# Kernel tuning notes

Measured on AMD Instinct MI355X. Metric: run time of the kernel, lower is better.

The kernel has to match this reference:

```python
import jax, jax.numpy as jnp
import numpy as np

NUM_USERS = 50000
NUM_FOODS = 20000
USER_FEAT_DIM = 256
FOOD_FEAT_DIM = 256
EMBED_DIM = 128
NUM_LAYERS = 3
NUM_HEADS = 4
THRESHOLD = 0.3
E_UF = 600000  # user->food interactions; symmetrized to 2*E_UF directed edges


def setup_inputs() -> dict:
    key = jax.random.key(0)
    ks = jax.random.split(key, 12)
    user_feat = jax.random.normal(ks[0], (NUM_USERS, USER_FEAT_DIM), jnp.float32)
    food_feat = jax.random.normal(ks[1], (NUM_FOODS, FOOD_FEAT_DIM), jnp.float32)
    # bipartite edges in global index space, symmetrized (both directions)
    u = jax.random.randint(ks[2], (E_UF,), 0, NUM_USERS)
    f = jax.random.randint(ks[3], (E_UF,), 0, NUM_FOODS) + NUM_USERS
    edge_index = jnp.stack([jnp.concatenate([u, f]), jnp.concatenate([f, u])]).astype(jnp.int64)
    s = 0.02
    W_user = jax.random.normal(ks[4], (USER_FEAT_DIM, EMBED_DIM), jnp.float32) * s
    b_user = jnp.zeros((EMBED_DIM,), jnp.float32)
    W_food = jax.random.normal(ks[5], (FOOD_FEAT_DIM, EMBED_DIM), jnp.float32) * s
    b_food = jnp.zeros((EMBED_DIM,), jnp.float32)
    Wq = jax.random.normal(ks[6], (EMBED_DIM, EMBED_DIM), jnp.float32) * s
    Wk = jax.random.normal(ks[7], (EMBED_DIM, EMBED_DIM), jnp.float32) * s
    channel_weights = jnp.zeros((2,), jnp.float32)  # StructurePooling fusion weights
    user_embed = jax.random.normal(ks[8], (NUM_USERS, EMBED_DIM), jnp.float32) * 0.1
    item_embed = jax.random.normal(ks[9], (NUM_FOODS, EMBED_DIM), jnp.float32) * 0.1
    return {"user_feat": user_feat, "food_feat": food_feat, "edge_index": edge_index,
            "W_user": W_user, "b_user": b_user, "W_food": W_food, "b_food": b_food,
            "Wq": Wq, "Wk": Wk, "channel_weights": channel_weights,
            "user_embed": user_embed, "item_embed": item_embed}


def reference(user_feat, food_feat, edge_index, W_user, b_user, W_food, b_food,
              Wq, Wk, channel_weights, user_embed, item_embed):
    N = NUM_USERS + NUM_FOODS
    Dh = EMBED_DIM // NUM_HEADS
    # feature projections + relu
    user_emb = jax.nn.relu(user_feat @ W_user + b_user)   # [U, D]
    food_emb = jax.nn.relu(food_feat @ W_food + b_food)   # [F, D]
    row, col = edge_index[0], edge_index[1]
    # graph generator: per-edge multi-head cosine similarity between user/food endpoints
    u_idx = jnp.where(row < NUM_USERS, row, col)
    f_idx = jnp.where(row < NUM_USERS, col, row) - NUM_USERS
    q = (user_emb[u_idx] @ Wq).reshape(-1, NUM_HEADS, Dh)  # [E, H, Dh]
    k = (food_emb[f_idx] @ Wk).reshape(-1, NUM_HEADS, Dh)
    eps = 1e-8
    sim = (q * k).sum(-1) / (jnp.linalg.norm(q, axis=-1) * jnp.linalg.norm(k, axis=-1) + eps)
    mask_feature = (sim.mean(-1) > THRESHOLD).astype(jnp.float32)  # [E]
    # structure pooling fusion of [all-ones, feature mask]
    w = jax.nn.softmax(channel_weights)
    fused = w[0] * 1.0 + w[1] * mask_feature
    edge_mask = (fused > 0.5).astype(jnp.float32)
    # LightGCN: symmetric-normalized propagation on the masked graph
    deg = jnp.maximum(jax.ops.segment_sum(edge_mask, row, num_segments=N), 1.0)
    norm = edge_mask / jnp.sqrt(deg[row] * deg[col])       # [E]
    x0 = jnp.concatenate([user_embed, item_embed], axis=0)  # [N, D]
    x = x0
    acc = x0
    for _ in range(NUM_LAYERS):
        x = jax.ops.segment_sum(norm[:, None] * x[col], row, num_segments=N)
        acc = acc + x
    out = acc / float(NUM_LAYERS + 1)
    return (out[:NUM_USERS], out[NUM_USERS:], user_embed, item_embed)
```

## Files before the change

kernel.cpp:

```cpp
#include <hip/hip_runtime.h>
#include <cstdint>

#define U_NUM 50000
#define F_NUM 20000
#define N_NUM 70000
#define D_EMB 128
#define THRESH 0.3f

typedef _Float16 half8 __attribute__((ext_vector_type(8)));
typedef float f32x4 __attribute__((ext_vector_type(4)));
typedef unsigned short u16x8 __attribute__((ext_vector_type(8)));

#define NRT_U ((U_NUM + 127) / 128)
#define NRT_F ((F_NUM + 127) / 128)
#define GRID_U (((NRT_U + 7) / 8) * 16)
#define GRID_F (((NRT_F + 7) / 8) * 16)

__device__ __forceinline__ void map_tile(int lb, int nRT, int& rt, int& ch, bool& valid)
{
    int g = lb >> 4, o = lb & 15;
    ch = (o >> 3) & 1;
    rt = g * 8 + (o & 7);
    valid = (rt < nRT);
}

__device__ __forceinline__ void gl_lds16(const void* g, void* l)
{
    __builtin_amdgcn_global_load_lds(
        (const __attribute__((address_space(1))) unsigned int*)g,
        (__attribute__((address_space(3))) unsigned int*)l, 16, 0, 0);
}

__global__ void presplit_zero(const float* __restrict__ Wu, const float* __restrict__ Wf,
                              const float* __restrict__ Wq, const float* __restrict__ Wk,
                              unsigned short* __restrict__ dst,
                              int* __restrict__ cnt, int* __restrict__ cursor)
{
    int i = blockIdx.x * 256 + threadIdx.x;
    if (i < N_NUM) { cnt[i] = 0; cursor[i] = 0; }
    if (i >= 98304) return;
    float a; size_t d; int pstride;
    if (i < 32768) {
        int n = i >> 8, k = i & 255;
        a = Wu[k * 128 + n]; d = (size_t)n * 256 + k; pstride = 32768;
    } else if (i < 65536) {
        int j = i - 32768; int n = j >> 8, k = j & 255;
        a = Wf[k * 128 + n]; d = 65536 + (size_t)n * 256 + k; pstride = 32768;
    } else if (i < 81920) {
        int j = i - 65536; int n = j >> 7, k = j & 127;
        a = Wq[k * 128 + n]; d = 131072 + (size_t)n * 128 + k; pstride = 16384;
    } else {
        int j = i - 81920; int n = j >> 7, k = j & 127;
        a = Wk[k * 128 + n]; d = 163840 + (size_t)n * 128 + k; pstride = 16384;
    }
    _Float16 c1 = (_Float16)a;
    float r = a - (float)c1;
    _Float16 c2 = (_Float16)r;
    dst[d]           = __builtin_bit_cast(unsigned short, c1);
    dst[d + pstride] = __builtin_bit_cast(unsigned short, c2);
}

__device__ __forceinline__ void split2v(const f32x4 x0, const f32x4 x1,
                                        half8& h, half8& lo)
{
    float v[8] = {x0[0], x0[1], x0[2], x0[3], x1[0], x1[1], x1[2], x1[3]};
#pragma unroll
    for (int i = 0; i < 8; i++) {
        _Float16 c1 = (_Float16)v[i];
        h[i] = c1;
        lo[i] = (_Float16)(v[i] - (float)c1);
    }
}

__global__ __launch_bounds__(256, 3)
void gemm1(const float* __restrict__ uf, const float* __restrict__ ff,
           const unsigned short* __restrict__ Wsp,
           const float* __restrict__ bu, const float* __restrict__ bfo,
           unsigned short* __restrict__ Eh)
{
    __shared__ char lds[49152];

    unsigned short* El = Eh + (size_t)N_NUM * 128;
    const int bid = blockIdx.x;
    const bool isU = bid < GRID_U;
    const int lb = isU ? bid : bid - GRID_U;
    int rt, chf; bool valid;
    map_tile(lb, isU ? NRT_U : NRT_F, rt, chf, valid);
    if (!valid) return;
    const int n0 = chf * 64;
    const int Mloc = isU ? U_NUM : F_NUM;
    const int combBase = isU ? 0 : U_NUM;
    const float* A  = isU ? uf : ff;
    const float* b1 = isU ? bu : bfo;
    const unsigned short* W = Wsp + (isU ? 0 : 65536);

    const int tid = threadIdx.x;
    const int w  = tid >> 6;
    const int l  = tid & 63;
    const int lm = l & 15;
    const int lq = l >> 4;
    const int wr = w * 32;

    auto stage = [&](int b, int kc) {
#pragma unroll
        for (int j = 0; j < 4; ++j) {
            int off = w * 4096 + j * 1024 + l * 16;
            int row = off >> 7;
            int ch  = (off & 127) >> 4;
            int gch = ch ^ (row & 7);
            int gr  = min(rt * 128 + row, Mloc - 1);
            const float* src = A + (size_t)gr * 256 + kc * 32 + gch * 4;
            gl_lds16(src, lds + b * 16384 + w * 4096 + j * 1024);
        }
#pragma unroll
        for (int j = 0; j < 2; ++j) {
            int off = w * 2048 + j * 1024 + l * 16;
            int p   = off >> 12;
            int n   = (off & 4095) >> 6;
            int ch  = (off & 63) >> 4;
            int gch = ch ^ ((n >> 1) & 3);
            const unsigned short* src = W + (size_t)p * 32768 + (size_t)(n0 + n) * 256 + kc * 32 + gch * 8;
            gl_lds16(src, lds + 32768 + b * 8192 + w * 2048 + j * 1024);
        }
    };

    stage(0, 0);
    __syncthreads();

    f32x4 acc[2][4];
#pragma unroll
    for (int i = 0; i < 2; i++)
#pragma unroll
        for (int j = 0; j < 4; j++) acc[i][j] = (f32x4)0.f;

    int buf = 0;
#pragma unroll
    for (int kc = 0; kc < 8; ++kc) {
        if (kc < 7) stage(buf ^ 1, kc + 1);

        half8 ah[2], al[2];
#pragma unroll
        for (int rb = 0; rb < 2; ++rb) {
            int lr = wr + rb * 16 + lm;
            int r7 = lr & 7;
            const float* basep = (const float*)(lds + buf * 16384 + lr * 128);
            f32x4 x0 = *(const f32x4*)(basep + ((((lq * 2)     ) ^ r7) << 2));
            f32x4 x1 = *(const f32x4*)(basep + ((((lq * 2) + 1) ^ r7) << 2));
            split2v(x0, x1, ah[rb], al[rb]);
        }
#pragma unroll
        for (int cb = 0; cb < 4; ++cb) {
            int n = cb * 16 + lm;
            int wc = lq ^ ((n >> 1) & 3);
            const char* wbase = lds + 32768 + buf * 8192;
            half8 bh = *(const half8*)(wbase + n * 64 + wc * 16);
            half8 bl = *(const half8*)(wbase + 4096 + n * 64 + wc * 16);
#pragma unroll
            for (int rb = 0; rb < 2; ++rb) {
                acc[rb][cb] = __builtin_amdgcn_mfma_f32_16x16x32_f16(al[rb], bh, acc[rb][cb], 0, 0, 0);
                acc[rb][cb] = __builtin_amdgcn_mfma_f32_16x16x32_f16(ah[rb], bl, acc[rb][cb], 0, 0, 0);
                acc[rb][cb] = __builtin_amdgcn_mfma_f32_16x16x32_f16(ah[rb], bh, acc[rb][cb], 0, 0, 0);
            }
        }
        __syncthreads();
        buf ^= 1;
    }

#pragma unroll
    for (int cb = 0; cb < 4; ++cb) {
        const int col = n0 + cb * 16 + lm;
        const float bb = b1[col];
#pragma unroll
        for (int rb = 0; rb < 2; ++rb)
#pragma unroll
            for (int rg = 0; rg < 4; ++rg) {
                int lr = wr + rb * 16 + lq * 4 + rg;
                if (rt * 128 + lr < Mloc) {
                    size_t rr = (size_t)(combBase + rt * 128 + lr);
                    float e = fmaxf(acc[rb][cb][rg] + bb, 0.f);
                    _Float16 c1 = (_Float16)e;
                    _Float16 c2 = (_Float16)(e - (float)c1);
                    Eh[rr * 128 + col] = __builtin_bit_cast(unsigned short, c1);
                    El[rr * 128 + col] = __builtin_bit_cast(unsigned short, c2);
                }
            }
    }
}

__global__ __launch_bounds__(256, 3)
void gemm2(const unsigned short* __restrict__ Eh,
           const unsigned short* __restrict__ Wsp,
           float* __restrict__ Qo, unsigned short* __restrict__ QKh)
{
    __shared__ char lds[49152];

    const unsigned short* El = Eh + (size_t)N_NUM * 128;
    const int bid = blockIdx.x;
    const bool isU = bid < GRID_U;
    const int lb = isU ? bid : bid - GRID_U;
    int rt, chf; bool valid;
    map_tile(lb, isU ? NRT_U : NRT_F, rt, chf, valid);
    if (!valid) return;
    const int n0 = chf * 64;
    const int Mloc = isU ? U_NUM : F_NUM;
    const int combBase = isU ? 0 : U_NUM;
    const unsigned short* W = Wsp + (isU ? 131072 : 163840);

    const int tid = threadIdx.x;
    const int w  = tid >> 6;
    const int l  = tid & 63;
    const int lm = l & 15;
    const int lq = l >> 4;
    const int wr = w * 32;

    auto stage = [&](int b, int kc) {
#pragma unroll
        for (int j = 0; j < 4; ++j) {
            int off = w * 4096 + j * 1024 + l * 16;
            int p   = off >> 13;
            int ro  = (off & 8191) >> 6;
            int ch  = (off & 63) >> 4;
            int gch = ch ^ ((ro >> 1) & 3);
            int gr  = min(rt * 128 + ro, Mloc - 1) + combBase;
            const unsigned short* src = (p ? El : Eh) + (size_t)gr * 128 + kc * 32 + gch * 8;
            gl_lds16(src, lds + b * 16384 + w * 4096 + j * 1024);
        }
#pragma unroll
        for (int j = 0; j < 2; ++j) {
            int off = w * 2048 + j * 1024 + l * 16;
            int p   = off >> 12;
            int n   = (off & 4095) >> 6;
            int ch  = (off & 63) >> 4;
            int gch = ch ^ ((n >> 1) & 3);
            const unsigned short* src = W + (size_t)p * 16384 + (size_t)(n0 + n) * 128 + kc * 32 + gch * 8;
            gl_lds16(src, lds + 32768 + b * 8192 + w * 2048 + j * 1024);
        }
    };

    stage(0, 0);
    __syncthreads();

    f32x4 acc[2][4];
#pragma unroll
    for (int i = 0; i < 2; i++)
#pragma unroll
        for (int j = 0; j < 4; j++) acc[i][j] = (f32x4)0.f;

    int buf = 0;
#pragma unroll
    for (int kc = 0; kc < 4; ++kc) {
        if (kc < 3) stage(buf ^ 1, kc + 1);

        half8 ah[2], al[2];
#pragma unroll
        for (int rb = 0; rb < 2; ++rb) {
            int lr = wr + rb * 16 + lm;
            int ech = lq ^ ((lr >> 1) & 3);
            const char* eb = lds + buf * 16384;
            ah[rb] = *(const half8*)(eb + lr * 64 + ech * 16);
            al[rb] = *(const half8*)(eb + 8192 + lr * 64 + ech * 16);
        }
#pragma unroll
        for (int cb = 0; cb < 4; ++cb) {
            int n = cb * 16 + lm;
            int wc = lq ^ ((n >> 1) & 3);
            const char* wbase = lds + 32768 + buf * 8192;
            half8 bh = *(const half8*)(wbase + n * 64 + wc * 16);
            half8 bl = *(const half8*)(wbase + 4096 + n * 64 + wc * 16);
#pragma unroll
            for (int rb = 0; rb < 2; ++rb) {
                acc[rb][cb] = __builtin_amdgcn_mfma_f32_16x16x32_f16(al[rb], bh, acc[rb][cb], 0, 0, 0);
                acc[rb][cb] = __builtin_amdgcn_mfma_f32_16x16x32_f16(ah[rb], bl, acc[rb][cb], 0, 0, 0);
                acc[rb][cb] = __builtin_amdgcn_mfma_f32_16x16x32_f16(ah[rb], bh, acc[rb][cb], 0, 0, 0);
            }
        }
        __syncthreads();
        buf ^= 1;
    }

#pragma unroll
    for (int cb = 0; cb < 4; ++cb) {
        const int col = n0 + cb * 16 + lm;
#pragma unroll
        for (int rb = 0; rb < 2; ++rb)
#pragma unroll
            for (int rg = 0; rg < 4; ++rg) {
                int lr = wr + rb * 16 + lq * 4 + rg;
                if (rt * 128 + lr < Mloc) {
                    size_t rr = (size_t)(combBase + rt * 128 + lr);
                    float v = acc[rb][cb][rg];
                    Qo[rr * 128 + col] = v;
                    QKh[rr * 128 + col] = __builtin_bit_cast(unsigned short, (_Float16)v);
                }
            }
    }
}

__global__ __launch_bounds__(256)
void edge_kernel(const int* __restrict__ ei, int Edir,
                 const unsigned short* __restrict__ QKh, const float* __restrict__ QKf,
                 const float* __restrict__ cwts,
                 float* __restrict__ maskf, int* __restrict__ cnt, int Eund)
{
    int gid = blockIdx.x * 256 + threadIdx.x;
    int e = gid >> 3;
    if (e >= Eund) return;
    int sub = gid & 7;
    int row = ei[e];
    int col = ei[Edir + e];
    row = min(max(row, 0), N_NUM - 1);
    col = min(max(col, 0), N_NUM - 1);
    int u  = (row < U_NUM) ? row : col;
    int fg = (row < U_NUM) ? col : row;
    u = min(max(u, 0), U_NUM - 1);
    int f = min(max(fg - U_NUM, 0), F_NUM - 1);
    const size_t qrow = (size_t)u * D_EMB;
    const size_t krow = (size_t)(U_NUM + f) * D_EMB;

    const unsigned short* qh = QKh + qrow + sub * 16;
    const unsigned short* kh = QKh + krow + sub * 16;
    u16x8 qa = *(const u16x8*)(qh);
    u16x8 qb = *(const u16x8*)(qh + 8);
    u16x8 ka = *(const u16x8*)(kh);
    u16x8 kb = *(const u16x8*)(kh + 8);
    float dot = 0.f, qq = 0.f, kk = 0.f;
#pragma unroll
    for (int i = 0; i < 8; i++) {
        float qv = (float)__builtin_bit_cast(_Float16, (unsigned short)qa[i]);
        float kv = (float)__builtin_bit_cast(_Float16, (unsigned short)ka[i]);
        dot += qv * kv; qq += qv * qv; kk += kv * kv;
    }
#pragma unroll
    for (int i = 0; i < 8; i++) {
        float qv = (float)__builtin_bit_cast(_Float16, (unsigned short)qb[i]);
        float kv = (float)__builtin_bit_cast(_Float16, (unsigned short)kb[i]);
        dot += qv * kv; qq += qv * qv; kk += kv * kv;
    }
    dot += __shfl_xor(dot, 1);
    qq  += __shfl_xor(qq, 1);
    kk  += __shfl_xor(kk, 1);
    float denom = sqrtf(qq) * sqrtf(kk) + 1e-8f;
    float sim = dot / denom;
    float s = sim + __shfl_xor(sim, 2);
    s += __shfl_xor(s, 4);
    float mean = s * 0.25f;

    if (fabsf(mean - THRESH) < 0.03f) {
        const float4* qp = (const float4*)(QKf + qrow + sub * 16);
        const float4* kp = (const float4*)(QKf + krow + sub * 16);
        float dot2 = 0.f, qq2 = 0.f, kk2 = 0.f;
#pragma unroll
        for (int i = 0; i < 4; i++) {
            float4 a = qp[i]; float4 b = kp[i];
            dot2 += a.x * b.x + a.y * b.y + a.z * b.z + a.w * b.w;
            qq2  += a.x * a.x + a.y * a.y + a.z * a.z + a.w * a.w;
            kk2  += b.x * b.x + b.y * b.y + b.z * b.z + b.w * b.w;
        }
        dot2 += __shfl_xor(dot2, 1);
        qq2  += __shfl_xor(qq2, 1);
        kk2  += __shfl_xor(kk2, 1);
        float denom2 = sqrtf(qq2) * sqrtf(kk2) + 1e-8f;
        float sim2 = dot2 / denom2;
        float s2 = sim2 + __shfl_xor(sim2, 2);
        s2 += __shfl_xor(s2, 4);
        mean = s2 * 0.25f;
    }

    float mf = (mean > THRESH) ? 1.f : 0.f;
    float cw0 = cwts[0], cw1 = cwts[1];
    float mx = fmaxf(cw0, cw1);
    float e0 = expf(cw0 - mx), e1 = expf(cw1 - mx);
    float inv = 1.f / (e0 + e1);
    float fused = e0 * inv + (e1 * inv) * mf;
    float em = (fused > 0.5f) ? 1.f : 0.f;

    if (sub == 0) {
        maskf[e] = em;
        if (em != 0.f) {
            atomicAdd(&cnt[row], 1);
            atomicAdd(&cnt[col], 1);
        }
    }
}

__global__ void scan_part(const int* __restrict__ cnt, int* __restrict__ part, int n)
{
    __shared__ int sd[256];
    int b = blockIdx.x, t = threadIdx.x;
    int base = b * 1024;
    int s = 0;
#pragma unroll
    for (int j = 0; j < 4; j++) {
        int idx = base + t + j * 256;
        if (idx < n) s += cnt[idx];
    }
    sd[t] = s; __syncthreads();
    for (int d = 128; d > 0; d >>= 1) {
        if (t < d) sd[t] += sd[t + d];
        __syncthreads();
    }
    if (t == 0) part[b] = sd[0];
}

__global__ void scan_small(int* part, int nb)
{
    __shared__ int sd[256];
    int t = threadIdx.x;
    sd[t] = (t < nb) ? part[t] : 0;
    __syncthreads();
    for (int d = 1; d < 256; d <<= 1) {
        int x = (t >= d) ? sd[t - d] : 0;
        __syncthreads();
        sd[t] += x;
        __syncthreads();
    }
    if (t < nb) part[t] = (t > 0) ? sd[t - 1] : 0;
}

__global__ void scan_final(const int* __restrict__ cnt, const int* __restrict__ part,
                           int* __restrict__ offs, int n)
{
    __shared__ int sd[256];
    int b = blockIdx.x, t = threadIdx.x;
    int base = b * 1024 + t * 4;
    int v[4]; int s = 0;
#pragma unroll
    for (int j = 0; j < 4; j++) {
        int idx = base + j;
        v[j] = (idx < n) ? cnt[idx] : 0;
        s += v[j];
    }
    sd[t] = s; __syncthreads();
    for (int d = 1; d < 256; d <<= 1) {
        int x = (t >= d) ? sd[t - d] : 0;
        __syncthreads();
        sd[t] += x;
        __syncthreads();
    }
    int prefix = part[b] + ((t > 0) ? sd[t - 1] : 0);
#pragma unroll
    for (int j = 0; j < 4; j++) {
        int idx = base + j;
        if (idx < n) offs[idx] = prefix;
        prefix += v[j];
    }
}

__global__ void scatter_kernel(const int* __restrict__ ei, int Edir,
                               const float* __restrict__ maskf,
                               const int* __restrict__ cnt, const int* __restrict__ offs,
                               int* __restrict__ cursor,
                               int* __restrict__ cnbr, float* __restrict__ cwA, int Eund)
{
    int e = blockIdx.x * 256 + threadIdx.x;
    if (e >= Eund) return;
    if (maskf[e] == 0.f) return;
    int row = ei[e], col = ei[Edir + e];
    row = min(max(row, 0), N_NUM - 1);
    col = min(max(col, 0), N_NUM - 1);
    float w = 1.0f / sqrtf((float)cnt[row] * (float)cnt[col]);
    int p1 = offs[row] + atomicAdd(&cursor[row], 1);
    cnbr[p1] = col; cwA[p1] = w;
    int p2 = offs[col] + atomicAdd(&cursor[col], 1);
    cnbr[p2] = row; cwA[p2] = w;
}

template<int MODE>
__global__ __launch_bounds__(256)
void prop(const int* __restrict__ offs, const int* __restrict__ cnt,
          const int* __restrict__ cnbr, const float* __restrict__ cwA,
          const float* __restrict__ xin,
          const float* __restrict__ ue, const float* __restrict__ ie,
          const float* __restrict__ x1b, float* __restrict__ xout,
          float* __restrict__ tail)
{
    int wid = (blockIdx.x << 2) + (threadIdx.x >> 6);
    if (wid >= N_NUM) return;
    int lane = threadIdx.x & 63;
    int num = cnt[wid];
    if (MODE != 2 && num == 0) return;
    int start = (num > 0) ? offs[wid] : 0;
    float ax = 0.f, ay = 0.f;

    auto srcp = [&](int c) -> const float* {
        if (MODE == 0)
            return (c < U_NUM) ? (ue + (size_t)c * D_EMB) : (ie + (size_t)(c - U_NUM) * D_EMB);
        else
            return xin + (size_t)c * D_EMB;
    };

    int j = 0;
    for (; j + 4 <= num; j += 4) {
        int c0i = cnbr[start + j],     c1i = cnbr[start + j + 1];
        int c2i = cnbr[start + j + 2], c3i = cnbr[start + j + 3];
        float w0 = cwA[start + j],     w1 = cwA[start + j + 1];
        float w2 = cwA[start + j + 2], w3 = cwA[start + j + 3];
        float2 v0 = *(const float2*)(srcp(c0i) + lane * 2);
        float2 v1 = *(const float2*)(srcp(c1i) + lane * 2);
        float2 v2 = *(const float2*)(srcp(c2i) + lane * 2);
        float2 v3 = *(const float2*)(srcp(c3i) + lane * 2);
        ax += w0 * v0.x; ay += w0 * v0.y;
        ax += w1 * v1.x; ay += w1 * v1.y;
        ax += w2 * v2.x; ay += w2 * v2.y;
        ax += w3 * v3.x; ay += w3 * v3.y;
    }
    for (; j < num; ++j) {
        int c = cnbr[start + j]; float w = cwA[start + j];
        float2 v = *(const float2*)(srcp(c) + lane * 2);
        ax += w * v.x; ay += w * v.y;
    }

    size_t o = (size_t)wid * D_EMB + lane * 2;
    if (MODE == 2) {
        const float* x0p = (wid < U_NUM) ? (ue + (size_t)wid * D_EMB)
                                         : (ie + (size_t)(wid - U_NUM) * D_EMB);
        float2 x0v = *(const float2*)(x0p + lane * 2);
        *(float2*)(tail + o) = x0v;
        float ox, oy;
        if (num == 0) {
            ox = x0v.x * 0.25f; oy = x0v.y * 0.25f;
        } else {
            float2 x1v = *(const float2*)(x1b + o);
            float2 x2v = *(const float2*)(xin + o);
            ox = ((x0v.x + x1v.x) + x2v.x + ax) * 0.25f;
            oy = ((x0v.y + x1v.y) + x2v.y + ay) * 0.25f;
        }
        *(float2*)(xout + o) = make_float2(ox, oy);
    } else {
        *(float2*)(xout + o) = make_float2(ax, ay);
    }
}

extern "C" void kernel_launch(void* const* d_in, const int* in_sizes, int n_in,
                              void* d_out, int out_size, void* d_ws, size_t ws_size,
                              hipStream_t stream)
{
    const float* user_feat  = (const float*)d_in[0];
    const float* food_feat  = (const float*)d_in[1];
    const int*   ei         = (const int*)d_in[2];
    const float* W_user     = (const float*)d_in[3];
    const float* b_user     = (const float*)d_in[4];
    const float* W_food     = (const float*)d_in[5];
    const float* b_food     = (const float*)d_in[6];
    const float* Wq         = (const float*)d_in[7];
    const float* Wk         = (const float*)d_in[8];
    const float* cwts       = (const float*)d_in[9];
    const float* user_embed = (const float*)d_in[10];
    const float* item_embed = (const float*)d_in[11];

    const int Edir = in_sizes[2] / 2;
    const int Eund = Edir / 2;

    char* ws = (char*)d_ws;
    size_t off = 0;
    auto alloc = [&](size_t nb) { size_t o = off; off += (nb + 255) & ~(size_t)255; return o; };

    float* Q     = (float*)(ws + alloc((size_t)N_NUM * D_EMB * 4));
    float* xB    = (float*)(ws + alloc((size_t)N_NUM * D_EMB * 4));
    unsigned short* QKh = (unsigned short*)(ws + alloc((size_t)N_NUM * D_EMB * 2));
    float* maskf = (float*)(ws + alloc((size_t)Eund * 4));
    int*   cnt   = (int*)  (ws + alloc((size_t)N_NUM * 4));
    int*   offs  = (int*)  (ws + alloc((size_t)N_NUM * 4));
    int*   cursor= (int*)  (ws + alloc((size_t)N_NUM * 4));
    int*   cnbr  = (int*)  (ws + alloc((size_t)Edir * 4));
    float* cwA   = (float*)(ws + alloc((size_t)Edir * 4));
    int*   part  = (int*)  (ws + alloc((size_t)256 * 4));
    unsigned short* Wsp = (unsigned short*)(ws + alloc((size_t)196608 * 2));
    (void)ws_size; (void)n_in; (void)out_size;

    float* xA = Q;
    unsigned short* Ehl = (unsigned short*)xB;

    presplit_zero<<<384, 256, 0, stream>>>(W_user, W_food, Wq, Wk, Wsp, cnt, cursor);

    gemm1<<<GRID_U + GRID_F, 256, 0, stream>>>(user_feat, food_feat, Wsp,
                                               b_user, b_food, Ehl);
    gemm2<<<GRID_U + GRID_F, 256, 0, stream>>>(Ehl, Wsp, Q, QKh);

    edge_kernel<<<(Eund * 8 + 255) / 256, 256, 0, stream>>>(ei, Edir, QKh, Q, cwts,
                                                            maskf, cnt, Eund);

    int nb = (N_NUM + 1023) / 1024;
    scan_part <<<nb, 256, 0, stream>>>(cnt, part, N_NUM);
    scan_small<<<1, 256, 0, stream>>>(part, nb);
    scan_final<<<nb, 256, 0, stream>>>(cnt, part, offs, N_NUM);

    scatter_kernel<<<(Eund + 255) / 256, 256, 0, stream>>>(ei, Edir, maskf, cnt, offs,
                                                           cursor, cnbr, cwA, Eund);

    int pb = (N_NUM + 3) / 4;
    float* tail = (float*)d_out + (size_t)N_NUM * D_EMB;
    prop<0><<<pb, 256, 0, stream>>>(offs, cnt, cnbr, cwA, nullptr, user_embed, item_embed,
                                    nullptr, xB, nullptr);
    prop<1><<<pb, 256, 0, stream>>>(offs, cnt, cnbr, cwA, xB, user_embed, item_embed,
                                    nullptr, xA, nullptr);
    prop<2><<<pb, 256, 0, stream>>>(offs, cnt, cnbr, cwA, xA, user_embed, item_embed,
                                    xB, (float*)d_out, tail);
}
```

Before: 150.1 us.

## Triple-buffer LDS staging in gemm1/gemm2 with vmcnt-based barriers

Both projection GEMMs move from double to triple buffering, prefetching two K-chunks ahead. Each iteration now waits with an explicit s_waitcnt vmcnt plus a barrier rather than a full __syncthreads, so loads for the next two stages can stay in flight during compute. The cost is more LDS per block (72KB), which drops the occupancy target from 3 to 2 blocks per CU. The vmcnt counts assume six outstanding loads per stage, so correctness depends on the compiler not reordering or merging those loads.

```diff
diff --git a/kernel.cpp b/kernel.cpp
--- a/kernel.cpp
+++ b/kernel.cpp
@@ -72,13 +72,19 @@
     }
 }
 
-__global__ __launch_bounds__(256, 3)
+#define VMCNT_BAR(n)                                             \
+    do {                                                         \
+        asm volatile("s_waitcnt vmcnt(" #n ")" ::: "memory");    \
+        __builtin_amdgcn_s_barrier();                            \
+    } while (0)
+
+__global__ __launch_bounds__(256, 2)
 void gemm1(const float* __restrict__ uf, const float* __restrict__ ff,
            const unsigned short* __restrict__ Wsp,
            const float* __restrict__ bu, const float* __restrict__ bfo,
            unsigned short* __restrict__ Eh)
 {
-    __shared__ char lds[49152];
+    __shared__ char lds[73728];
 
     unsigned short* El = Eh + (size_t)N_NUM * 128;
     const int bid = blockIdx.x;
@@ -120,23 +126,24 @@
             int ch  = (off & 63) >> 4;
             int gch = ch ^ ((n >> 1) & 3);
             const unsigned short* src = W + (size_t)p * 32768 + (size_t)(n0 + n) * 256 + kc * 32 + gch * 8;
-            gl_lds16(src, lds + 32768 + b * 8192 + w * 2048 + j * 1024);
+            gl_lds16(src, lds + 49152 + b * 8192 + w * 2048 + j * 1024);
         }
     };
 
+    f32x4 acc[2][4];
+#pragma unroll
+    for (int i = 0; i < 2; i++)
+#pragma unroll
+        for (int j = 0; j < 4; j++) acc[i][j] = (f32x4)0.f;
+
     stage(0, 0);
-    __syncthreads();
-
-    f32x4 acc[2][4];
-#pragma unroll
-    for (int i = 0; i < 2; i++)
-#pragma unroll
-        for (int j = 0; j < 4; j++) acc[i][j] = (f32x4)0.f;
-
-    int buf = 0;
+    stage(1, 1);
+    VMCNT_BAR(6);
+
 #pragma unroll
     for (int kc = 0; kc < 8; ++kc) {
-        if (kc < 7) stage(buf ^ 1, kc + 1);
+        if (kc + 2 < 8) stage((kc + 2) % 3, kc + 2);
+        const int buf = kc % 3;
 
         half8 ah[2], al[2];
 #pragma unroll
@@ -144,7 +151,7 @@
             int lr = wr + rb * 16 + lm;
             int r7 = lr & 7;
             const float* basep = (const float*)(lds + buf * 16384 + lr * 128);
-            f32x4 x0 = *(const f32x4*)(basep + ((((lq * 2)     ) ^ r7) << 2));
+            f32x4 x0 = *(const f32x4*)(basep + ((((lq * 2)    ) ^ r7) << 2));
             f32x4 x1 = *(const f32x4*)(basep + ((((lq * 2) + 1) ^ r7) << 2));
             split2v(x0, x1, ah[rb], al[rb]);
         }
@@ -152,7 +159,7 @@
         for (int cb = 0; cb < 4; ++cb) {
             int n = cb * 16 + lm;
             int wc = lq ^ ((n >> 1) & 3);
-            const char* wbase = lds + 32768 + buf * 8192;
+            const char* wbase = lds + 49152 + buf * 8192;
             half8 bh = *(const half8*)(wbase + n * 64 + wc * 16);
             half8 bl = *(const half8*)(wbase + 4096 + n * 64 + wc * 16);
 #pragma unroll
@@ -162,8 +169,11 @@
                 acc[rb][cb] = __builtin_amdgcn_mfma_f32_16x16x32_f16(ah[rb], bh, acc[rb][cb], 0, 0, 0);
             }
         }
-        __syncthreads();
-        buf ^= 1;
+
+        if (kc < 7) {
+            if (kc + 2 < 8) { VMCNT_BAR(6); }
+            else           { VMCNT_BAR(0); }
+        }
     }
 
 #pragma unroll
@@ -187,12 +197,12 @@
     }
 }
 
-__global__ __launch_bounds__(256, 3)
+__global__ __launch_bounds__(256, 2)
 void gemm2(const unsigned short* __restrict__ Eh,
            const unsigned short* __restrict__ Wsp,
            float* __restrict__ Qo, unsigned short* __restrict__ QKh)
 {
-    __shared__ char lds[49152];
+    __shared__ char lds[73728];
 
     const unsigned short* El = Eh + (size_t)N_NUM * 128;
     const int bid = blockIdx.x;
@@ -233,23 +243,24 @@
             int ch  = (off & 63) >> 4;
             int gch = ch ^ ((n >> 1) & 3);
             const unsigned short* src = W + (size_t)p * 16384 + (size_t)(n0 + n) * 128 + kc * 32 + gch * 8;
-            gl_lds16(src, lds + 32768 + b * 8192 + w * 2048 + j * 1024);
+            gl_lds16(src, lds + 49152 + b * 8192 + w * 2048 + j * 1024);
         }
     };
 
+    f32x4 acc[2][4];
+#pragma unroll
+    for (int i = 0; i < 2; i++)
+#pragma unroll
+        for (int j = 0; j < 4; j++) acc[i][j] = (f32x4)0.f;
+
     stage(0, 0);
-    __syncthreads();
-
-    f32x4 acc[2][4];
-#pragma unroll
-    for (int i = 0; i < 2; i++)
-#pragma unroll
-        for (int j = 0; j < 4; j++) acc[i][j] = (f32x4)0.f;
-
-    int buf = 0;
+    stage(1, 1);
+    VMCNT_BAR(6);
+
 #pragma unroll
     for (int kc = 0; kc < 4; ++kc) {
-        if (kc < 3) stage(buf ^ 1, kc + 1);
+        if (kc + 2 < 4) stage((kc + 2) % 3, kc + 2);
+        const int buf = kc % 3;
 
         half8 ah[2], al[2];
 #pragma unroll
@@ -264,7 +275,7 @@
         for (int cb = 0; cb < 4; ++cb) {
             int n = cb * 16 + lm;
             int wc = lq ^ ((n >> 1) & 3);
-            const char* wbase = lds + 32768 + buf * 8192;
+            const char* wbase = lds + 49152 + buf * 8192;
             half8 bh = *(const half8*)(wbase + n * 64 + wc * 16);
             half8 bl = *(const half8*)(wbase + 4096 + n * 64 + wc * 16);
 #pragma unroll
@@ -274,8 +285,11 @@
                 acc[rb][cb] = __builtin_amdgcn_mfma_f32_16x16x32_f16(ah[rb], bh, acc[rb][cb], 0, 0, 0);
             }
         }
-        __syncthreads();
-        buf ^= 1;
+
+        if (kc < 3) {
+            if (kc + 2 < 4) { VMCNT_BAR(6); }
+            else           { VMCNT_BAR(0); }
+        }
     }
 
 #pragma unroll
```

Measured after the change: 152.4 us. No clear change (+1.6%).

## Widen GEMM tiles to full 128 output columns per block

Applied to the files above, without the earlier changes.

Both projection GEMMs now compute all 128 output columns in one block instead of splitting them into two 64-column halves across blocks. Each A row tile is then loaded and split into fp16 hi/lo parts only once, which removes the duplicated A-tile global reads and conversion work. In exchange, LDS per block rises to 64KB, the accumulator register count doubles, launch bounds drop to 2 blocks per SM, and the grid is halved. This lowers occupancy and leaves fewer blocks to spread across the CUs.

```diff
diff --git a/kernel.cpp b/kernel.cpp
--- a/kernel.cpp
+++ b/kernel.cpp
@@ -13,16 +13,6 @@
 
 #define NRT_U ((U_NUM + 127) / 128)
 #define NRT_F ((F_NUM + 127) / 128)
-#define GRID_U (((NRT_U + 7) / 8) * 16)
-#define GRID_F (((NRT_F + 7) / 8) * 16)
-
-__device__ __forceinline__ void map_tile(int lb, int nRT, int& rt, int& ch, bool& valid)
-{
-    int g = lb >> 4, o = lb & 15;
-    ch = (o >> 3) & 1;
-    rt = g * 8 + (o & 7);
-    valid = (rt < nRT);
-}
 
 __device__ __forceinline__ void gl_lds16(const void* g, void* l)
 {
@@ -72,22 +62,18 @@
     }
 }
 
-__global__ __launch_bounds__(256, 3)
+__global__ __launch_bounds__(256, 2)
 void gemm1(const float* __restrict__ uf, const float* __restrict__ ff,
            const unsigned short* __restrict__ Wsp,
            const float* __restrict__ bu, const float* __restrict__ bfo,
            unsigned short* __restrict__ Eh)
 {
-    __shared__ char lds[49152];
+    __shared__ char lds[65536];
 
     unsigned short* El = Eh + (size_t)N_NUM * 128;
     const int bid = blockIdx.x;
-    const bool isU = bid < GRID_U;
-    const int lb = isU ? bid : bid - GRID_U;
-    int rt, chf; bool valid;
-    map_tile(lb, isU ? NRT_U : NRT_F, rt, chf, valid);
-    if (!valid) return;
-    const int n0 = chf * 64;
+    const bool isU = bid < NRT_U;
+    const int rt = isU ? bid : bid - NRT_U;
     const int Mloc = isU ? U_NUM : F_NUM;
     const int combBase = isU ? 0 : U_NUM;
     const float* A  = isU ? uf : ff;
@@ -113,25 +99,25 @@
             gl_lds16(src, lds + b * 16384 + w * 4096 + j * 1024);
         }
 #pragma unroll
-        for (int j = 0; j < 2; ++j) {
-            int off = w * 2048 + j * 1024 + l * 16;
-            int p   = off >> 12;
-            int n   = (off & 4095) >> 6;
+        for (int j = 0; j < 4; ++j) {
+            int off = w * 4096 + j * 1024 + l * 16;
+            int p   = off >> 13;
+            int n   = (off & 8191) >> 6;
             int ch  = (off & 63) >> 4;
             int gch = ch ^ ((n >> 1) & 3);
-            const unsigned short* src = W + (size_t)p * 32768 + (size_t)(n0 + n) * 256 + kc * 32 + gch * 8;
-            gl_lds16(src, lds + 32768 + b * 8192 + w * 2048 + j * 1024);
+            const unsigned short* src = W + (size_t)p * 32768 + (size_t)n * 256 + kc * 32 + gch * 8;
+            gl_lds16(src, lds + 32768 + b * 16384 + w * 4096 + j * 1024);
         }
     };
 
     stage(0, 0);
     __syncthreads();
 
-    f32x4 acc[2][4];
+    f32x4 acc[2][8];
 #pragma unroll
     for (int i = 0; i < 2; i++)
 #pragma unroll
-        for (int j = 0; j < 4; j++) acc[i][j] = (f32x4)0.f;
+        for (int j = 0; j < 8; j++) acc[i][j] = (f32x4)0.f;
 
     int buf = 0;
 #pragma unroll
@@ -144,17 +130,17 @@
             int lr = wr + rb * 16 + lm;
             int r7 = lr & 7;
             const float* basep = (const float*)(lds + buf * 16384 + lr * 128);
-            f32x4 x0 = *(const f32x4*)(basep + ((((lq * 2)     ) ^ r7) << 2));
+            f32x4 x0 = *(const f32x4*)(basep + ((((lq * 2)    ) ^ r7) << 2));
             f32x4 x1 = *(const f32x4*)(basep + ((((lq * 2) + 1) ^ r7) << 2));
             split2v(x0, x1, ah[rb], al[rb]);
         }
 #pragma unroll
-        for (int cb = 0; cb < 4; ++cb) {
+        for (int cb = 0; cb < 8; ++cb) {
             int n = cb * 16 + lm;
             int wc = lq ^ ((n >> 1) & 3);
-            const char* wbase = lds + 32768 + buf * 8192;
+            const char* wbase = lds + 32768 + buf * 16384;
             half8 bh = *(const half8*)(wbase + n * 64 + wc * 16);
-            half8 bl = *(const half8*)(wbase + 4096 + n * 64 + wc * 16);
+            half8 bl = *(const half8*)(wbase + 8192 + n * 64 + wc * 16);
 #pragma unroll
             for (int rb = 0; rb < 2; ++rb) {
                 acc[rb][cb] = __builtin_amdgcn_mfma_f32_16x16x32_f16(al[rb], bh, acc[rb][cb], 0, 0, 0);
@@ -167,8 +153,8 @@
     }
 
 #pragma unroll
-    for (int cb = 0; cb < 4; ++cb) {
-        const int col = n0 + cb * 16 + lm;
+    for (int cb = 0; cb < 8; ++cb) {
+        const int col = cb * 16 + lm;
         const float bb = b1[col];
 #pragma unroll
         for (int rb = 0; rb < 2; ++rb)
@@ -187,21 +173,17 @@
     }
 }
 
-__global__ __launch_bounds__(256, 3)
+__global__ __launch_bounds__(256, 2)
 void gemm2(const unsigned short* __restrict__ Eh,
            const unsigned short* __restrict__ Wsp,
            float* __restrict__ Qo, unsigned short* __restrict__ QKh)
 {
-    __shared__ char lds[49152];
+    __shared__ char lds[65536];
 
     const unsigned short* El = Eh + (size_t)N_NUM * 128;
     const int bid = blockIdx.x;
-    const bool isU = bid < GRID_U;
-    const int lb = isU ? bid : bid - GRID_U;
-    int rt, chf; bool valid;
-    map_tile(lb, isU ? NRT_U : NRT_F, rt, chf, valid);
-    if (!valid) return;
-    const int n0 = chf * 64;
+    const bool isU = bid < NRT_U;
+    const int rt = isU ? bid : bid - NRT_U;
     const int Mloc = isU ? U_NUM : F_NUM;
     const int combBase = isU ? 0 : U_NUM;
     const unsigned short* W = Wsp + (isU ? 131072 : 163840);
@@ -226,25 +208,25 @@
             gl_lds16(src, lds + b * 16384 + w * 4096 + j * 1024);
         }
 #pragma unroll
-        for (int j = 0; j < 2; ++j) {
-            int off = w * 2048 + j * 1024 + l * 16;
-            int p   = off >> 12;
-            int n   = (off & 4095) >> 6;
+        for (int j = 0; j < 4; ++j) {
+            int off = w * 4096 + j * 1024 + l * 16;
+            int p   = off >> 13;
+            int n   = (off & 8191) >> 6;
             int ch  = (off & 63) >> 4;
             int gch = ch ^ ((n >> 1) & 3);
-            const unsigned short* src = W + (size_t)p * 16384 + (size_t)(n0 + n) * 128 + kc * 32 + gch * 8;
-            gl_lds16(src, lds + 32768 + b * 8192 + w * 2048 + j * 1024);
+            const unsigned short* src = W + (size_t)p * 16384 + (size_t)n * 128 + kc * 32 + gch * 8;
+            gl_lds16(src, lds + 32768 + b * 16384 + w * 4096 + j * 1024);
         }
     };
 
     stage(0, 0);
     __syncthreads();
 
-    f32x4 acc[2][4];
+    f32x4 acc[2][8];
 #pragma unroll
     for (int i = 0; i < 2; i++)
 #pragma unroll
-        for (int j = 0; j < 4; j++) acc[i][j] = (f32x4)0.f;
+        for (int j = 0; j < 8; j++) acc[i][j] = (f32x4)0.f;
 
     int buf = 0;
 #pragma unroll
@@ -261,12 +243,12 @@
             al[rb] = *(const half8*)(eb + 8192 + lr * 64 + ech * 16);
         }
 #pragma unroll
-        for (int cb = 0; cb < 4; ++cb) {
+        for (int cb = 0; cb < 8; ++cb) {
             int n = cb * 16 + lm;
             int wc = lq ^ ((n >> 1) & 3);
-            const char* wbase = lds + 32768 + buf * 8192;
+            const char* wbase = lds + 32768 + buf * 16384;
             half8 bh = *(const half8*)(wbase + n * 64 + wc * 16);
-            half8 bl = *(const half8*)(wbase + 4096 + n * 64 + wc * 16);
+            half8 bl = *(const half8*)(wbase + 8192 + n * 64 + wc * 16);
 #pragma unroll
             for (int rb = 0; rb < 2; ++rb) {
                 acc[rb][cb] = __builtin_amdgcn_mfma_f32_16x16x32_f16(al[rb], bh, acc[rb][cb], 0, 0, 0);
@@ -279,8 +261,8 @@
     }
 
 #pragma unroll
-    for (int cb = 0; cb < 4; ++cb) {
-        const int col = n0 + cb * 16 + lm;
+    for (int cb = 0; cb < 8; ++cb) {
+        const int col = cb * 16 + lm;
 #pragma unroll
         for (int rb = 0; rb < 2; ++rb)
 #pragma unroll
@@ -573,9 +555,9 @@
 
     presplit_zero<<<384, 256, 0, stream>>>(W_user, W_food, Wq, Wk, Wsp, cnt, cursor);
 
-    gemm1<<<GRID_U + GRID_F, 256, 0, stream>>>(user_feat, food_feat, Wsp,
-                                               b_user, b_food, Ehl);
-    gemm2<<<GRID_U + GRID_F, 256, 0, stream>>>(Ehl, Wsp, Q, QKh);
+    gemm1<<<NRT_U + NRT_F, 256, 0, stream>>>(user_feat, food_feat, Wsp,
+                                             b_user, b_food, Ehl);
+    gemm2<<<NRT_U + NRT_F, 256, 0, stream>>>(Ehl, Wsp, Q, QKh);
 
     edge_kernel<<<(Eund * 8 + 255) / 256, 256, 0, stream>>>(ei, Edir, QKh, Q, cwts,
                                                             maskf, cnt, Eund);
```

Result: slower. 164.3 us (+9.5%).
